# Kernel tuning notes

Measured on AMD Instinct MI355X. Metric: run time of the kernel, lower is better.

The kernel has to match this reference:

```python
import jax, jax.numpy as jnp
import numpy as np

N, E = 50000, 1000000
IN_DIM, HID, OUT = 2, 32, 16
H1, H2 = 4, 1
NEG_SLOPE = 0.2
LN_EPS = 1e-5


def _glorot(key, shape):
    fan_in, fan_out = shape[0], shape[1]
    lim = (6.0 / (fan_in + fan_out)) ** 0.5
    return jax.random.uniform(key, shape, jnp.float32, -lim, lim)


def layer_norm(x, g, b):
    mu = jnp.mean(x, axis=-1, keepdims=True)
    var = jnp.var(x, axis=-1, keepdims=True)
    return (x - mu) * jax.lax.rsqrt(var + LN_EPS) * g + b


def gatv2_conv(x, src, dst, edge_attr, Wl, bl, Wr, br, We, att, bias, H, C):
    # x: (N, F) -> out: (N, C)  (concat=False: mean over heads)
    n = x.shape[0]
    xl = (x @ Wl + bl).reshape(n, H, C)   # source transform
    xr = (x @ Wr + br).reshape(n, H, C)   # destination transform
    e = (edge_attr @ We).reshape(-1, H, C)  # edge feature transform (no bias)
    # per-edge message, LeakyReLU, attention logit
    m = jax.nn.leaky_relu(xl[src] + xr[dst] + e, NEG_SLOPE)  # (E, H, C)
    logit = jnp.einsum('ehc,hc->eh', m, att)                 # (E, H)
    # scatter softmax grouped by destination node
    amax = jax.ops.segment_max(logit, dst, num_segments=n)    # (N, H)
    ex = jnp.exp(logit - amax[dst])                           # (E, H)
    denom = jax.ops.segment_sum(ex, dst, num_segments=n)      # (N, H)
    alpha = ex / (denom[dst] + 1e-16)                         # (E, H)
    # weighted scatter-aggregate of source features
    out = jax.ops.segment_sum(alpha[:, :, None] * xl[src], dst, num_segments=n)  # (N, H, C)
    return jnp.mean(out, axis=1) + bias


def setup_inputs() -> dict:
    key = jax.random.key(0)
    ks = jax.random.split(key, 16)
    x = jax.random.normal(ks[0], (N, IN_DIM), jnp.float32)
    edge_index = jax.random.randint(ks[1], (2, E), 0, N, jnp.int64)
    edge_attr = jax.random.normal(ks[2], (E, 1), jnp.float32)
    inp = {
        'x': x, 'edge_index': edge_index, 'edge_attr': edge_attr,
        # layer 1 (in=2 -> H1*HID)
        'W1l': _glorot(ks[3], (IN_DIM, H1 * HID)), 'b1l': jnp.zeros((H1 * HID,), jnp.float32),
        'W1r': _glorot(ks[4], (IN_DIM, H1 * HID)), 'b1r': jnp.zeros((H1 * HID,), jnp.float32),
        'We1': _glorot(ks[5], (1, H1 * HID)),
        'att1': _glorot(ks[6], (H1, HID)),
        'bias1': jnp.zeros((HID,), jnp.float32),
        'g1': jnp.ones((HID,), jnp.float32), 'beta1': jnp.zeros((HID,), jnp.float32),
        # layer 2 (HID -> H2*OUT)
        'W2l': _glorot(ks[7], (HID, H2 * OUT)), 'b2l': jnp.zeros((H2 * OUT,), jnp.float32),
        'W2r': _glorot(ks[8], (HID, H2 * OUT)), 'b2r': jnp.zeros((H2 * OUT,), jnp.float32),
        'We2': _glorot(ks[9], (1, H2 * OUT)),
        'att2': _glorot(ks[10], (H2, OUT)),
        'bias2': jnp.zeros((OUT,), jnp.float32),
        'g2': jnp.ones((OUT,), jnp.float32), 'beta2': jnp.zeros((OUT,), jnp.float32),
    }
    return inp


def reference(x, edge_index, edge_attr, W1l, b1l, W1r, b1r, We1, att1, bias1, g1, beta1,
              W2l, b2l, W2r, b2r, We2, att2, bias2, g2, beta2):
    src, dst = edge_index[0], edge_index[1]
    h = gatv2_conv(x, src, dst, edge_attr, W1l, b1l, W1r, b1r, We1, att1, bias1, H1, HID)
    h = jax.nn.elu(layer_norm(h, g1, beta1))  # dropout p=0.0 -> identity
    z = gatv2_conv(h, src, dst, edge_attr, W2l, b2l, W2r, b2r, We2, att2, bias2, H2, OUT)
    return layer_norm(z, g2, beta2)
```

## Files before the change

kernel.cpp:

```cpp
#include <hip/hip_runtime.h>
#include <hip/hip_bf16.h>
#include <math.h>

typedef __hip_bfloat16 bf16;

__device__ __forceinline__ float b2f(bf16 v) { return __bfloat162float(v); }
__device__ __forceinline__ bf16  f2b(float v) { return __float2bfloat16(v); }

template<int F32>
__device__ __forceinline__ float ldf(const void* p, int i) {
    return F32 ? ((const float*)p)[i] : b2f(((const bf16*)p)[i]);
}
template<int F32>
__device__ __forceinline__ void ldx(const void* x, int s, float& x0, float& x1) {
    if (F32) { float2 v = ((const float2*)x)[s]; x0 = v.x; x1 = v.y; }
    else {
        unsigned u = ((const unsigned*)x)[s];
        x0 = __uint_as_float((u & 0xFFFFu) << 16);
        x1 = __uint_as_float(u & 0xFFFF0000u);
    }
}
__device__ __forceinline__ unsigned f2b_hi(float f) {
    unsigned u = __float_as_uint(f);
    u += 0x7FFFu + ((u >> 16) & 1u);
    return u & 0xFFFF0000u;
}
template<int P4>
__device__ __forceinline__ void ldrec(const void* csr, int k, int& s, float& a) {
    if (P4) {
        unsigned u = ((const unsigned*)csr)[k];
        s = (int)(u & 0xFFFFu);
        a = __uint_as_float(u & 0xFFFF0000u);
    } else {
        uint2 r = ((const uint2*)csr)[k];
        s = (int)r.x;
        a = __uint_as_float(r.y);
    }
}
__device__ __forceinline__ float sclamp(float v, float lim) {
    return fminf(fmaxf(v, -lim), lim);
}
template<int CTRL>
__device__ __forceinline__ float dpp_add(float v) {
    int t = __builtin_amdgcn_update_dpp(0, __float_as_int(v), CTRL, 0xF, 0xF, true);
    return v + __int_as_float(t);
}
__device__ __forceinline__ float red16(float v) {
    v = dpp_add<0xB1>(v);
    v = dpp_add<0x4E>(v);
    v = dpp_add<0x124>(v);
    v = dpp_add<0x128>(v);
    return v;
}

#define NEG_SLOPE 0.2f
#define LN_EPS 1e-5f
#define SCAN_TILE 1024
#define ACHUNK 2048
#define EBMAX 512

__device__ __forceinline__ int ld_idx(const int* ei, long long pos, int is64, int N) {
    int v = is64 ? ei[2 * pos] : ei[pos];
    return min(max(v, 0), N - 1);
}
__device__ __forceinline__ int calc_is64(const int* ei) {
    int hi = 0, nz = 0;
    #pragma unroll
    for (int i = 0; i < 8; ++i) { hi |= ei[2 * i + 1]; nz |= ei[2 * i]; }
    return (hi == 0 && nz != 0) ? 1 : 0;
}
__device__ __forceinline__ int calc_isf32(const unsigned short* xu) {
    int pl = 0;
    for (int i = 0; i < 32; ++i) {
        unsigned ex = (xu[2 * i] >> 7) & 0xFF;
        if (ex >= 100 && ex <= 140) pl++;
    }
    return (pl >= 24) ? 0 : 1;
}


template<int F32>
__device__ void bina1_body(const int* __restrict__ ei, const void* __restrict__ attr,
                           int E, int N, int is64,
                           uint2* __restrict__ binned, int* __restrict__ cntm,
                           int* __restrict__ locm,
                           int* cnt, int* incl, int* cur, uint2* stage) {
    int tid = threadIdx.x, b = blockIdx.x;
    cnt[tid] = 0;
    __syncthreads();
    int i0 = b * ACHUNK;
    int iend = min(i0 + ACHUNK, E);
    uint2 rec[8]; int bk[8];
    #pragma unroll
    for (int r = 0; r < 8; ++r) {
        int i = i0 + tid + r * 256;
        bk[r] = -1;
        if (i < iend) {
            int d = ld_idx(ei, (long long)E + i, is64, N);
            int s = ld_idx(ei, (long long)i, is64, N);
            float a = ldf<F32>(attr, i);
            rec[r] = make_uint2((unsigned)s | ((unsigned)(d & 255) << 16), f2b_hi(a));
            bk[r] = d >> 8;
            atomicAdd(&cnt[bk[r]], 1);
        }
    }
    __syncthreads();
    incl[tid] = cnt[tid];
    __syncthreads();
    for (int off = 1; off < 256; off <<= 1) {
        int u = (tid >= off) ? incl[tid - off] : 0;
        __syncthreads();
        incl[tid] += u;
        __syncthreads();
    }
    cur[tid] = incl[tid] - cnt[tid];
    __syncthreads();
    #pragma unroll
    for (int r = 0; r < 8; ++r) {
        if (bk[r] >= 0) {
            int p = atomicAdd(&cur[bk[r]], 1);
            stage[p] = rec[r];
        }
    }
    __syncthreads();
    int n = iend - i0;
    for (int i = tid; i < n; i += 256)
        binned[(size_t)b * ACHUNK + i] = stage[i];
    cntm[b * 256 + tid] = cnt[tid];
    locm[b * 256 + tid] = incl[tid] - cnt[tid];
}

__global__ __launch_bounds__(256) void bina1_kernel(const int* __restrict__ ei,
                                                    const void* __restrict__ attr,
                                                    const unsigned short* __restrict__ xu,
                                                    int E, int N, int* __restrict__ flags,
                                                    uint2* __restrict__ binned,
                                                    int* __restrict__ cntm,
                                                    int* __restrict__ locm) {
    __shared__ int cnt[256], incl[256], cur[256];
    __shared__ uint2 stage[ACHUNK];
    __shared__ int sflags[2];
    if (threadIdx.x == 0) {
        sflags[0] = calc_is64(ei);
        sflags[1] = calc_isf32(xu);
        if (blockIdx.x == 0) { flags[0] = sflags[0]; flags[1] = sflags[1]; }
    }
    __syncthreads();
    if (sflags[1]) bina1_body<1>(ei, attr, E, N, sflags[0], binned, cntm, locm,
                                 cnt, incl, cur, stage);
    else           bina1_body<0>(ei, attr, E, N, sflags[0], binned, cntm, locm,
                                 cnt, incl, cur, stage);
}

__global__ __launch_bounds__(256) void sumb_kernel(const int* __restrict__ cntm,
                                                   int* __restrict__ btot, int EB) {
    __shared__ int w[4];
    int B = blockIdx.x, tid = threadIdx.x;
    int s = 0;
    for (int j = tid; j < EB; j += 256) s += cntm[j * 256 + B];
    #pragma unroll
    for (int off = 1; off < 64; off <<= 1) s += __shfl_xor(s, off);
    if ((tid & 63) == 0) w[tid >> 6] = s;
    __syncthreads();
    if (tid == 0) btot[B] = w[0] + w[1] + w[2] + w[3];
}

__global__ void scanc_kernel(const int* __restrict__ btot, int* __restrict__ bbase,
                             int* __restrict__ rowptr, int NB, int N, int E) {
    __shared__ int s[256];
    int tid = threadIdx.x;
    int v = (tid < NB) ? btot[tid] : 0;
    s[tid] = v;
    __syncthreads();
    for (int off = 1; off < 256; off <<= 1) {
        int u = (tid >= off) ? s[tid - off] : 0;
        __syncthreads();
        s[tid] += u;
        __syncthreads();
    }
    if (tid < NB) bbase[tid] = s[tid] - v;
    if (tid == 0) { bbase[NB] = s[255]; rowptr[N] = E; }
}

__global__ __launch_bounds__(256) void passb_kernel(const uint2* __restrict__ binned,
                                                    const int* __restrict__ cntm,
                                                    const int* __restrict__ locm,
                                                    const int* __restrict__ bbase,
                                                    int* __restrict__ rowptr,
                                                    unsigned* __restrict__ csr,
                                                    int N, int EB) {
    __shared__ int nc[256], incl[256], cur[256];
    __shared__ int cntl[EBMAX], locl[EBMAX];
    int B = blockIdx.x, tid = threadIdx.x;
    for (int j = tid; j < EB; j += 256) {
        cntl[j] = cntm[j * 256 + B];
        locl[j] = locm[j * 256 + B];
    }
    nc[tid] = 0;
    __syncthreads();
    for (int j = tid; j < EB; j += 256) {
        int c = cntl[j];
        const uint2* src = binned + (size_t)j * ACHUNK + locl[j];
        for (int i = 0; i < c; ++i)
            atomicAdd(&nc[(src[i].x >> 16) & 255], 1);
    }
    __syncthreads();
    incl[tid] = nc[tid];
    __syncthreads();
    for (int off = 1; off < 256; off <<= 1) {
        int u = (tid >= off) ? incl[tid - off] : 0;
        __syncthreads();
        incl[tid] += u;
        __syncthreads();
    }
    int base = bbase[B];
    int excl = incl[tid] - nc[tid];
    int node = (B << 8) + tid;
    if (node < N) rowptr[node] = base + excl;
    cur[tid] = excl;
    __syncthreads();
    for (int j = tid; j < EB; j += 256) {
        int c = cntl[j];
        const uint2* src = binned + (size_t)j * ACHUNK + locl[j];
        for (int i = 0; i < c; ++i) {
            uint2 r = src[i];
            int p = atomicAdd(&cur[(r.x >> 16) & 255], 1);
            csr[base + p] = r.y | (r.x & 0xFFFFu);
        }
    }
}


__global__ void hist_kernel(const int* __restrict__ ei, const unsigned short* __restrict__ xu,
                            int E, int N, int* __restrict__ flags, int* __restrict__ cnt) {
    int is64 = calc_is64(ei);
    if (blockIdx.x == 0 && threadIdx.x == 0) {
        flags[0] = is64;
        flags[1] = calc_isf32(xu);
    }
    int e = blockIdx.x * blockDim.x + threadIdx.x;
    if (e >= E) return;
    atomicAdd(&cnt[ld_idx(ei, (long long)E + e, is64, N)], 1);
}

__global__ __launch_bounds__(256) void scan_partial(const int* __restrict__ cnt,
                                                    int* __restrict__ bsum, int N) {
    __shared__ int wsum[4];
    int b = blockIdx.x, tid = threadIdx.x;
    int base = b * SCAN_TILE + tid * 4;
    int4 v = make_int4(0, 0, 0, 0);
    if (base + 3 < N) v = *(const int4*)(cnt + base);
    else {
        if (base + 0 < N) v.x = cnt[base + 0];
        if (base + 1 < N) v.y = cnt[base + 1];
        if (base + 2 < N) v.z = cnt[base + 2];
    }
    int s = v.x + v.y + v.z + v.w;
    #pragma unroll
    for (int off = 1; off < 64; off <<= 1) s += __shfl_xor(s, off);
    if ((tid & 63) == 0) wsum[tid >> 6] = s;
    __syncthreads();
    if (tid == 0) bsum[b] = wsum[0] + wsum[1] + wsum[2] + wsum[3];
}

__global__ __launch_bounds__(256) void scan_final(int* __restrict__ cnt, int* __restrict__ rowptr,
                                                  const int* __restrict__ bsum, int N, int B) {
    __shared__ int tsum[256];
    __shared__ int bpre[256];
    int b = blockIdx.x, tid = threadIdx.x;
    bpre[tid] = (tid < B) ? bsum[tid] : 0;
    int base = b * SCAN_TILE + tid * 4;
    int4 v = make_int4(0, 0, 0, 0);
    if (base + 3 < N) v = *(const int4*)(cnt + base);
    else {
        if (base + 0 < N) v.x = cnt[base + 0];
        if (base + 1 < N) v.y = cnt[base + 1];
        if (base + 2 < N) v.z = cnt[base + 2];
    }
    tsum[tid] = v.x + v.y + v.z + v.w;
    __syncthreads();
    for (int off = 1; off < 256; off <<= 1) {
        int t = (tid >= off) ? tsum[tid - off] : 0;
        int u = (tid >= off) ? bpre[tid - off] : 0;
        __syncthreads();
        tsum[tid] += t;
        bpre[tid] += u;
        __syncthreads();
    }
    int blockpre = (b == 0) ? 0 : bpre[b - 1];
    int o0 = blockpre + ((tid == 0) ? 0 : tsum[tid - 1]);
    int o1 = o0 + v.x, o2 = o1 + v.y, o3 = o2 + v.z;
    if (base + 3 < N) {
        int4 o = make_int4(o0, o1, o2, o3);
        *(int4*)(rowptr + base) = o;
        *(int4*)(cnt + base) = o;
    } else {
        if (base + 0 < N) { rowptr[base + 0] = o0; cnt[base + 0] = o0; }
        if (base + 1 < N) { rowptr[base + 1] = o1; cnt[base + 1] = o1; }
        if (base + 2 < N) { rowptr[base + 2] = o2; cnt[base + 2] = o2; }
    }
    if (b == 0 && tid == 255) rowptr[N] = bpre[255];
}

template<int F32>
__device__ void scatter_body(const int* __restrict__ ei, const void* __restrict__ attr,
                             int E, int N, int is64, int* __restrict__ cursor,
                             uint2* __restrict__ csr) {
    int e = blockIdx.x * blockDim.x + threadIdx.x;
    if (e >= E) return;
    int d = ld_idx(ei, (long long)E + e, is64, N);
    int s = ld_idx(ei, (long long)e, is64, N);
    float av = ldf<F32>(attr, e);
    int pos = atomicAdd(&cursor[d], 1);
    csr[pos] = make_uint2((unsigned)s, __float_as_uint(av));
}

__global__ void scatter_kernel(const int* __restrict__ ei, const void* __restrict__ attr,
                               int E, int N, const int* __restrict__ flags,
                               int* __restrict__ cursor, uint2* __restrict__ csr) {
    if (flags[1]) scatter_body<1>(ei, attr, E, N, flags[0], cursor, csr);
    else          scatter_body<0>(ei, attr, E, N, flags[0], cursor, csr);
}


template<int F32, int P4>
__device__ void agg1_body(
    const int* __restrict__ rowptr, const void* __restrict__ csr,
    const void* __restrict__ x,
    const void* W1l, const void* b1l, const void* W1r, const void* b1r,
    const void* We1, const void* att1, const void* bias1, const void* g1v, const void* beta1,
    bf16* __restrict__ hout, int N) {
    int w0 = __builtin_amdgcn_readfirstlane((blockIdx.x * blockDim.x + threadIdx.x) >> 6);
    int NW = (gridDim.x * blockDim.x) >> 6;
    int lane = threadIdx.x & 63;
    int h = lane >> 4, q = lane & 15;
    int ja = h * 32 + q, jb = ja + 16;

    float wlaA = ldf<F32>(W1l, ja),      wlaB = ldf<F32>(W1l, jb);
    float wlbA = ldf<F32>(W1l, 128 + ja), wlbB = ldf<F32>(W1l, 128 + jb);
    float wraA = ldf<F32>(W1r, ja),      wraB = ldf<F32>(W1r, jb);
    float wrbA = ldf<F32>(W1r, 128 + ja), wrbB = ldf<F32>(W1r, 128 + jb);
    float blA = ldf<F32>(b1l, ja), blB = ldf<F32>(b1l, jb);
    float brA = ldf<F32>(b1r, ja), brB = ldf<F32>(b1r, jb);
    float weA = ldf<F32>(We1, ja), weB = ldf<F32>(We1, jb);
    float atA = ldf<F32>(att1, ja), atB = ldf<F32>(att1, jb);
    float aa4A = 0.4f * atA, aa4B = 0.4f * atB;
    float blbrA = blA + brA, blbrB = blB + brB;
    float P0 = 0.6f * red16(atA * wlaA + atB * wlaB);
    float P1 = 0.6f * red16(atA * wlbA + atB * wlbB);
    float Pw = 0.6f * red16(atA * weA + atB * weB);
    float Q0 = 0.6f * red16(atA * wraA + atB * wraB);
    float Q1 = 0.6f * red16(atA * wrbA + atB * wrbB);
    float Qc = 0.6f * red16(atA * blbrA + atB * blbrB);
    float biasA = ldf<F32>(bias1, q), biasB = ldf<F32>(bias1, q + 16);
    float gA = ldf<F32>(g1v, q), gB = ldf<F32>(g1v, q + 16);
    float beA = ldf<F32>(beta1, q), beB = ldf<F32>(beta1, q + 16);

    for (int n = w0; n < N; n += NW) {
        int beg = rowptr[n], end = rowptr[n + 1];
        float xd0, xd1;
        ldx<F32>(x, n, xd0, xd1);
        float cA = fmaf(xd0, wraA, fmaf(xd1, wrbA, blbrA));
        float cB = fmaf(xd0, wraB, fmaf(xd1, wrbB, blbrB));
        float Kn = fmaf(xd0, Q0, fmaf(xd1, Q1, Qc));
        float S = 0.f, Sx0 = 0.f, Sx1 = 0.f;

        auto edge = [&](float xs0, float xs1, float a) {
            float zA = fmaf(xs0, wlaA, fmaf(xs1, wlbA, fmaf(a, weA, cA)));
            float zB = fmaf(xs0, wlaB, fmaf(xs1, wlbB, fmaf(a, weB, cB)));
            float pabs = red16(fmaf(fabsf(zA), aa4A, fabsf(zB) * aa4B));
            float p = sclamp(fmaf(xs0, P0, fmaf(xs1, P1, fmaf(a, Pw, Kn))) + pabs, 60.f);
            float e = __expf(p);
            S += e;
            Sx0 = fmaf(e, xs0, Sx0);
            Sx1 = fmaf(e, xs1, Sx1);
        };

        int k = beg;
        for (; k + 4 <= end; k += 4) {
            int s0, s1, s2, s3;
            float a0, a1, a2, a3;
            ldrec<P4>(csr, k, s0, a0);
            ldrec<P4>(csr, k + 1, s1, a1);
            ldrec<P4>(csr, k + 2, s2, a2);
            ldrec<P4>(csr, k + 3, s3, a3);
            float p0, p1, q0, q1, r0, r1, t0, t1;
            ldx<F32>(x, s0, p0, p1);
            ldx<F32>(x, s1, q0, q1);
            ldx<F32>(x, s2, r0, r1);
            ldx<F32>(x, s3, t0, t1);
            edge(p0, p1, a0);
            edge(q0, q1, a1);
            edge(r0, r1, a2);
            edge(t0, t1, a3);
        }
        for (; k < end; ++k) {
            int s0; float a0;
            ldrec<P4>(csr, k, s0, a0);
            float p0, p1;
            ldx<F32>(x, s0, p0, p1);
            edge(p0, p1, a0);
        }

        float inv = 1.0f / (S + 1e-16f);
        float R = S * inv, U0 = Sx0 * inv, U1 = Sx1 * inv;
        float outA = fmaf(U0, wlaA, fmaf(U1, wlbA, R * blA));
        float outB = fmaf(U0, wlaB, fmaf(U1, wlbB, R * blB));
        outA += __shfl_xor(outA, 16); outA += __shfl_xor(outA, 32);
        outB += __shfl_xor(outB, 16); outB += __shfl_xor(outB, 32);
        float valA = fmaf(0.25f, outA, biasA);
        float valB = fmaf(0.25f, outB, biasB);
        float mu = red16(valA + valB) * (1.f / 32.f);
        float dA = valA - mu, dB = valB - mu;
        float var = red16(dA * dA + dB * dB) * (1.f / 32.f);
        float rs = rsqrtf(var + LN_EPS);
        float yA = fmaf(dA * rs, gA, beA);
        float yB = fmaf(dB * rs, gB, beB);
        float hA = yA > 0.f ? yA : expm1f(yA);
        float hB = yB > 0.f ? yB : expm1f(yB);
        if (lane < 16) {
            hout[n * 32 + q]      = f2b(hA);
            hout[n * 32 + 16 + q] = f2b(hB);
        }
    }
}

template<int P4>
__global__ __launch_bounds__(256) void agg1_kernel(
    const int* __restrict__ flags,
    const int* __restrict__ rowptr, const void* __restrict__ csr,
    const void* __restrict__ x,
    const void* W1l, const void* b1l, const void* W1r, const void* b1r,
    const void* We1, const void* att1, const void* bias1, const void* g1v, const void* beta1,
    bf16* __restrict__ hout, int N) {
    if (flags[1]) agg1_body<1, P4>(rowptr, csr, x, W1l, b1l, W1r, b1r,
                                   We1, att1, bias1, g1v, beta1, hout, N);
    else          agg1_body<0, P4>(rowptr, csr, x, W1l, b1l, W1r, b1r,
                                   We1, att1, bias1, g1v, beta1, hout, N);
}


template<int F32>
__device__ void node2_body(bf16* __restrict__ hbuf, float* wl, float* wr,
                           const void* W2l, const void* b2l, const void* W2r, const void* b2r,
                           int N) {
    __shared__ float bl[16], br[16];
    int tid = threadIdx.x;
    for (int i = tid; i < 512; i += 256) { wl[i] = ldf<F32>(W2l, i); wr[i] = ldf<F32>(W2r, i); }
    if (tid < 16) { bl[tid] = ldf<F32>(b2l, tid); br[tid] = ldf<F32>(b2r, tid); }
    __syncthreads();
    int n = blockIdx.x * blockDim.x + tid;
    if (n >= N) return;
    float hv[32];
    #pragma unroll
    for (int c = 0; c < 32; ++c) hv[c] = b2f(hbuf[n * 32 + c]);
    float accl[16], accr[16];
    #pragma unroll
    for (int o = 0; o < 16; ++o) { accl[o] = bl[o]; accr[o] = br[o]; }
    #pragma unroll
    for (int c = 0; c < 32; ++c) {
        #pragma unroll
        for (int o = 0; o < 16; ++o) {
            accl[o] = fmaf(hv[c], wl[c * 16 + o], accl[o]);
            accr[o] = fmaf(hv[c], wr[c * 16 + o], accr[o]);
        }
    }
    #pragma unroll
    for (int o = 0; o < 16; ++o) {
        hbuf[n * 32 + o]      = f2b(accl[o]);
        hbuf[n * 32 + 16 + o] = f2b(accr[o]);
    }
}

__global__ __launch_bounds__(256) void node2_kernel(
    const int* __restrict__ flags, bf16* __restrict__ hbuf,
    const void* W2l, const void* b2l, const void* W2r, const void* b2r, int N) {
    __shared__ float wl[512], wr[512];
    if (flags[1]) node2_body<1>(hbuf, wl, wr, W2l, b2l, W2r, b2r, N);
    else          node2_body<0>(hbuf, wl, wr, W2l, b2l, W2r, b2r, N);
}


template<int F32, int P4>
__device__ void agg2_body(
    const int* __restrict__ rowptr, const void* __restrict__ csr,
    const bf16* __restrict__ h2,
    const void* We2, const void* att2, const void* bias2, const void* g2v, const void* beta2,
    void* __restrict__ out, int N) {
    int w0 = __builtin_amdgcn_readfirstlane((blockIdx.x * blockDim.x + threadIdx.x) >> 6);
    int NW = (gridDim.x * blockDim.x) >> 6;
    int lane = threadIdx.x & 63;
    int g = lane >> 4, t = lane & 15;

    float we = ldf<F32>(We2, t), at = ldf<F32>(att2, t);
    float bia = ldf<F32>(bias2, t), gg = ldf<F32>(g2v, t), bb = ldf<F32>(beta2, t);

    for (int n = w0; n < N; n += NW) {
        int beg = rowptr[n], end = rowptr[n + 1];
        float xr = b2f(h2[n * 32 + 16 + t]);

        float S = 0.f, A = 0.f;
        auto edge = [&](float v, float a) {
            float m = fmaf(a, we, v + xr);
            m = fmaxf(m, NEG_SLOPE * m);
            float p = sclamp(red16(m * at), 60.f);
            float e = __expf(p);
            S += e;
            A = fmaf(e, v, A);
        };
        int k = beg + g;
        for (; k + 4 < end; k += 8) {
            int s0, s1; float a0, a1;
            ldrec<P4>(csr, k, s0, a0);
            ldrec<P4>(csr, k + 4, s1, a1);
            float v0 = b2f(h2[s0 * 32 + t]);
            float v1 = b2f(h2[s1 * 32 + t]);
            edge(v0, a0);
            edge(v1, a1);
        }
        if (k < end) {
            int s0; float a0;
            ldrec<P4>(csr, k, s0, a0);
            edge(b2f(h2[s0 * 32 + t]), a0);
        }
        S += __shfl_xor(S, 16); S += __shfl_xor(S, 32);
        A += __shfl_xor(A, 16); A += __shfl_xor(A, 32);
        float val = A / (S + 1e-16f) + bia;

        float mu = red16(val) * (1.f / 16.f);
        float d = val - mu;
        float var = red16(d * d) * (1.f / 16.f);
        float y = fmaf(d * rsqrtf(var + LN_EPS), gg, bb);
        if (lane < 16) {
            if (F32) ((float*)out)[n * 16 + t] = y;
            else     ((bf16*)out)[n * 16 + t] = f2b(y);
        }
    }
}

template<int P4>
__global__ __launch_bounds__(256) void agg2_kernel(
    const int* __restrict__ flags,
    const int* __restrict__ rowptr, const void* __restrict__ csr,
    const bf16* __restrict__ h2,
    const void* We2, const void* att2, const void* bias2, const void* g2v, const void* beta2,
    void* __restrict__ out, int N) {
    if (flags[1]) agg2_body<1, P4>(rowptr, csr, h2, We2, att2, bias2, g2v, beta2, out, N);
    else          agg2_body<0, P4>(rowptr, csr, h2, We2, att2, bias2, g2v, beta2, out, N);
}


static inline size_t align256(size_t x) { return (x + 255) & ~size_t(255); }

extern "C" void kernel_launch(void* const* d_in, const int* in_sizes, int n_in,
                              void* d_out, int out_size, void* d_ws, size_t ws_size,
                              hipStream_t stream) {
    const void* x     = d_in[0];
    const int*  ei    = (const int*)d_in[1];
    const void* eattr = d_in[2];
    const void* W1l   = d_in[3];
    const void* b1l   = d_in[4];
    const void* W1r   = d_in[5];
    const void* b1r   = d_in[6];
    const void* We1   = d_in[7];
    const void* att1  = d_in[8];
    const void* bias1 = d_in[9];
    const void* g1    = d_in[10];
    const void* beta1 = d_in[11];
    const void* W2l   = d_in[12];
    const void* b2l   = d_in[13];
    const void* W2r   = d_in[14];
    const void* b2r   = d_in[15];
    const void* We2   = d_in[16];
    const void* att2  = d_in[17];
    const void* bias2 = d_in[18];
    const void* g2    = d_in[19];
    const void* beta2 = d_in[20];

    const int N = in_sizes[0] / 2;
    const int E = in_sizes[2];
    const int EB = (E + ACHUNK - 1) / ACHUNK;
    const int NB = (N + 255) >> 8;
    const bool p4 = (N <= 65536) && (EB <= EBMAX);

    char* ws = (char*)d_ws;
    size_t off = 0;
    int* flags  = (int*)(ws + off); off += align256(sizeof(int) * 2);
    int* cntm   = (int*)(ws + off); off += align256(sizeof(int) * (size_t)EB * 256);
    int* locm   = (int*)(ws + off); off += align256(sizeof(int) * (size_t)EB * 256);
    int* btot   = (int*)(ws + off); off += align256(sizeof(int) * 256);
    int* bbase  = (int*)(ws + off); off += align256(sizeof(int) * 257);
    int* rowptr = (int*)(ws + off); off += align256(sizeof(int) * (size_t)(N + 1));
    void* csr   = (void*)(ws + off); off += align256((p4 ? 4u : 8u) * (size_t)E);
    char* big   = (ws + off);
    uint2* binned = (uint2*)big;
    bf16*  hbuf   = (bf16*)big;

    if (p4) {
        bina1_kernel<<<EB, 256, 0, stream>>>(ei, eattr, (const unsigned short*)x,
                                             E, N, flags, binned, cntm, locm);
        sumb_kernel<<<NB, 256, 0, stream>>>(cntm, btot, EB);
        scanc_kernel<<<1, 256, 0, stream>>>(btot, bbase, rowptr, NB, N, E);
        passb_kernel<<<NB, 256, 0, stream>>>(binned, cntm, locm, bbase, rowptr,
                                             (unsigned*)csr, N, EB);
    } else {
        int* cnt = (int*)big;
        hbuf = (bf16*)(big + align256(sizeof(int) * (size_t)N));
        const int B = (N + SCAN_TILE - 1) / SCAN_TILE;
        hipMemsetAsync(cnt, 0, sizeof(int) * (size_t)N, stream);
        hist_kernel<<<(E + 255) / 256, 256, 0, stream>>>(ei, (const unsigned short*)x, E, N, flags, cnt);
        scan_partial<<<B, 256, 0, stream>>>(cnt, cntm, N);
        scan_final<<<B, 256, 0, stream>>>(cnt, rowptr, cntm, N, B);
        scatter_kernel<<<(E + 255) / 256, 256, 0, stream>>>(ei, eattr, E, N, flags, cnt, (uint2*)csr);
    }

    if (p4) agg1_kernel<1><<<2048, 256, 0, stream>>>(flags, rowptr, csr, x,
                                                     W1l, b1l, W1r, b1r, We1, att1,
                                                     bias1, g1, beta1, hbuf, N);
    else    agg1_kernel<0><<<2048, 256, 0, stream>>>(flags, rowptr, csr, x,
                                                     W1l, b1l, W1r, b1r, We1, att1,
                                                     bias1, g1, beta1, hbuf, N);

    node2_kernel<<<(N + 255) / 256, 256, 0, stream>>>(flags, hbuf, W2l, b2l, W2r, b2r, N);

    if (p4) agg2_kernel<1><<<2048, 256, 0, stream>>>(flags, rowptr, csr, hbuf,
                                                     We2, att2, bias2, g2, beta2, d_out, N);
    else    agg2_kernel<0><<<2048, 256, 0, stream>>>(flags, rowptr, csr, hbuf,
                                                     We2, att2, bias2, g2, beta2, d_out, N);
}
```

Before: 219.0 us.

## Split binned records into packed words plus byte keys and stage per-bucket in LDS

The intermediate binned edge records shrink from 8 bytes to a 4-byte packed source/attr word plus a separate 1-byte low-destination key. The single-block scan kernel is removed: each passb block now scans the bucket totals itself, and sumb writes rowptr[N]. When a bucket fits in shared memory (up to 8192 edges), passb reads its edges from global memory once into LDS and does the counting and final scatter from LDS, instead of reading the binned data twice. This cuts global traffic and one launch, at the cost of a larger LDS footprint per block and a fallback path for oversized buckets.

```diff
diff --git a/kernel.cpp b/kernel.cpp
--- a/kernel.cpp
+++ b/kernel.cpp
@@ -58,6 +58,7 @@
 #define SCAN_TILE 1024
 #define ACHUNK 2048
 #define EBMAX 512
+#define SCAP 8192
 
 __device__ __forceinline__ int ld_idx(const int* ei, long long pos, int is64, int N) {
     int v = is64 ? ei[2 * pos] : ei[pos];
@@ -82,15 +83,16 @@
 template<int F32>
 __device__ void bina1_body(const int* __restrict__ ei, const void* __restrict__ attr,
                            int E, int N, int is64,
-                           uint2* __restrict__ binned, int* __restrict__ cntm,
-                           int* __restrict__ locm,
-                           int* cnt, int* incl, int* cur, uint2* stage) {
+                           unsigned* __restrict__ binned4, unsigned char* __restrict__ binnedb,
+                           int* __restrict__ cntm, int* __restrict__ locm,
+                           int* cnt, int* incl, int* cur,
+                           unsigned* stage4, unsigned char* stageb) {
     int tid = threadIdx.x, b = blockIdx.x;
     cnt[tid] = 0;
     __syncthreads();
     int i0 = b * ACHUNK;
     int iend = min(i0 + ACHUNK, E);
-    uint2 rec[8]; int bk[8];
+    unsigned rec[8]; int bk[8], lo[8];
     #pragma unroll
     for (int r = 0; r < 8; ++r) {
         int i = i0 + tid + r * 256;
@@ -99,8 +101,9 @@
             int d = ld_idx(ei, (long long)E + i, is64, N);
             int s = ld_idx(ei, (long long)i, is64, N);
             float a = ldf<F32>(attr, i);
-            rec[r] = make_uint2((unsigned)s | ((unsigned)(d & 255) << 16), f2b_hi(a));
+            rec[r] = f2b_hi(a) | (unsigned)s;
             bk[r] = d >> 8;
+            lo[r] = d & 255;
             atomicAdd(&cnt[bk[r]], 1);
         }
     }
@@ -119,13 +122,16 @@
     for (int r = 0; r < 8; ++r) {
         if (bk[r] >= 0) {
             int p = atomicAdd(&cur[bk[r]], 1);
-            stage[p] = rec[r];
+            stage4[p] = rec[r];
+            stageb[p] = (unsigned char)lo[r];
         }
     }
     __syncthreads();
     int n = iend - i0;
-    for (int i = tid; i < n; i += 256)
-        binned[(size_t)b * ACHUNK + i] = stage[i];
+    for (int i = tid; i < n; i += 256) {
+        binned4[(size_t)b * ACHUNK + i] = stage4[i];
+        binnedb[(size_t)b * ACHUNK + i] = stageb[i];
+    }
     cntm[b * 256 + tid] = cnt[tid];
     locm[b * 256 + tid] = incl[tid] - cnt[tid];
 }
@@ -134,11 +140,13 @@
                                                     const void* __restrict__ attr,
                                                     const unsigned short* __restrict__ xu,
                                                     int E, int N, int* __restrict__ flags,
-                                                    uint2* __restrict__ binned,
+                                                    unsigned* __restrict__ binned4,
+                                                    unsigned char* __restrict__ binnedb,
                                                     int* __restrict__ cntm,
                                                     int* __restrict__ locm) {
     __shared__ int cnt[256], incl[256], cur[256];
-    __shared__ uint2 stage[ACHUNK];
+    __shared__ unsigned stage4[ACHUNK];
+    __shared__ unsigned char stageb[ACHUNK];
     __shared__ int sflags[2];
     if (threadIdx.x == 0) {
         sflags[0] = calc_is64(ei);
@@ -146,16 +154,18 @@
         if (blockIdx.x == 0) { flags[0] = sflags[0]; flags[1] = sflags[1]; }
     }
     __syncthreads();
-    if (sflags[1]) bina1_body<1>(ei, attr, E, N, sflags[0], binned, cntm, locm,
-                                 cnt, incl, cur, stage);
-    else           bina1_body<0>(ei, attr, E, N, sflags[0], binned, cntm, locm,
-                                 cnt, incl, cur, stage);
+    if (sflags[1]) bina1_body<1>(ei, attr, E, N, sflags[0], binned4, binnedb, cntm, locm,
+                                 cnt, incl, cur, stage4, stageb);
+    else           bina1_body<0>(ei, attr, E, N, sflags[0], binned4, binnedb, cntm, locm,
+                                 cnt, incl, cur, stage4, stageb);
 }
 
 __global__ __launch_bounds__(256) void sumb_kernel(const int* __restrict__ cntm,
-                                                   int* __restrict__ btot, int EB) {
+                                                   int* __restrict__ btot, int EB,
+                                                   int* __restrict__ rowptr, int N, int E) {
     __shared__ int w[4];
     int B = blockIdx.x, tid = threadIdx.x;
+    if (B == 0 && tid == 0) rowptr[N] = E;
     int s = 0;
     for (int j = tid; j < EB; j += 256) s += cntm[j * 256 + B];
     #pragma unroll
@@ -165,44 +175,63 @@
     if (tid == 0) btot[B] = w[0] + w[1] + w[2] + w[3];
 }
 
-__global__ void scanc_kernel(const int* __restrict__ btot, int* __restrict__ bbase,
-                             int* __restrict__ rowptr, int NB, int N, int E) {
-    __shared__ int s[256];
-    int tid = threadIdx.x;
-    int v = (tid < NB) ? btot[tid] : 0;
-    s[tid] = v;
-    __syncthreads();
-    for (int off = 1; off < 256; off <<= 1) {
-        int u = (tid >= off) ? s[tid - off] : 0;
-        __syncthreads();
-        s[tid] += u;
-        __syncthreads();
-    }
-    if (tid < NB) bbase[tid] = s[tid] - v;
-    if (tid == 0) { bbase[NB] = s[255]; rowptr[N] = E; }
-}
-
-__global__ __launch_bounds__(256) void passb_kernel(const uint2* __restrict__ binned,
+__global__ __launch_bounds__(256) void passb_kernel(const unsigned* __restrict__ binned4,
+                                                    const unsigned char* __restrict__ binnedb,
                                                     const int* __restrict__ cntm,
                                                     const int* __restrict__ locm,
-                                                    const int* __restrict__ bbase,
+                                                    const int* __restrict__ btot,
                                                     int* __restrict__ rowptr,
                                                     unsigned* __restrict__ csr,
-                                                    int N, int EB) {
-    __shared__ int nc[256], incl[256], cur[256];
+                                                    int N, int EB, int NB) {
+    __shared__ int nc[256], incl[256], cur[256], bsc[256], ebase[256];
     __shared__ int cntl[EBMAX], locl[EBMAX];
+    __shared__ unsigned stage4[SCAP];
+    __shared__ unsigned char stageb[SCAP];
+    __shared__ int stageCnt;
     int B = blockIdx.x, tid = threadIdx.x;
+    int v = (tid < NB) ? btot[tid] : 0;
+    bsc[tid] = v;
+    nc[tid] = 0;
+    if (tid == 0) stageCnt = 0;
     for (int j = tid; j < EB; j += 256) {
         cntl[j] = cntm[j * 256 + B];
         locl[j] = locm[j * 256 + B];
     }
-    nc[tid] = 0;
-    __syncthreads();
-    for (int j = tid; j < EB; j += 256) {
-        int c = cntl[j];
-        const uint2* src = binned + (size_t)j * ACHUNK + locl[j];
-        for (int i = 0; i < c; ++i)
-            atomicAdd(&nc[(src[i].x >> 16) & 255], 1);
+    __syncthreads();
+    for (int off = 1; off < 256; off <<= 1) {
+        int u = (tid >= off) ? bsc[tid - off] : 0;
+        __syncthreads();
+        bsc[tid] += u;
+        __syncthreads();
+    }
+    ebase[tid] = bsc[tid] - v;
+    __syncthreads();
+    int base = ebase[B];
+    int cntb = btot[B];
+    bool fit = (cntb <= SCAP);
+
+    if (fit) {
+        for (int j = tid; j < EB; j += 256) {
+            int c = cntl[j];
+            if (c > 0) {
+                int p = atomicAdd(&stageCnt, c);
+                const unsigned* s4 = binned4 + (size_t)j * ACHUNK + locl[j];
+                const unsigned char* sb = binnedb + (size_t)j * ACHUNK + locl[j];
+                for (int i = 0; i < c; ++i) {
+                    unsigned r4 = s4[i];
+                    unsigned char l = sb[i];
+                    stage4[p + i] = r4;
+                    stageb[p + i] = l;
+                    atomicAdd(&nc[l], 1);
+                }
+            }
+        }
+    } else {
+        for (int j = tid; j < EB; j += 256) {
+            int c = cntl[j];
+            const unsigned char* sb = binnedb + (size_t)j * ACHUNK + locl[j];
+            for (int i = 0; i < c; ++i) atomicAdd(&nc[sb[i]], 1);
+        }
     }
     __syncthreads();
     incl[tid] = nc[tid];
@@ -213,19 +242,26 @@
         incl[tid] += u;
         __syncthreads();
     }
-    int base = bbase[B];
     int excl = incl[tid] - nc[tid];
     int node = (B << 8) + tid;
     if (node < N) rowptr[node] = base + excl;
     cur[tid] = excl;
     __syncthreads();
-    for (int j = tid; j < EB; j += 256) {
-        int c = cntl[j];
-        const uint2* src = binned + (size_t)j * ACHUNK + locl[j];
-        for (int i = 0; i < c; ++i) {
-            uint2 r = src[i];
-            int p = atomicAdd(&cur[(r.x >> 16) & 255], 1);
-            csr[base + p] = r.y | (r.x & 0xFFFFu);
+    if (fit) {
+        for (int i = tid; i < cntb; i += 256) {
+            int l = stageb[i];
+            int p = atomicAdd(&cur[l], 1);
+            csr[base + p] = stage4[i];
+        }
+    } else {
+        for (int j = tid; j < EB; j += 256) {
+            int c = cntl[j];
+            const unsigned* s4 = binned4 + (size_t)j * ACHUNK + locl[j];
+            const unsigned char* sb = binnedb + (size_t)j * ACHUNK + locl[j];
+            for (int i = 0; i < c; ++i) {
+                int p = atomicAdd(&cur[sb[i]], 1);
+                csr[base + p] = s4[i];
+            }
         }
     }
 }
@@ -589,20 +625,19 @@
     int* cntm   = (int*)(ws + off); off += align256(sizeof(int) * (size_t)EB * 256);
     int* locm   = (int*)(ws + off); off += align256(sizeof(int) * (size_t)EB * 256);
     int* btot   = (int*)(ws + off); off += align256(sizeof(int) * 256);
-    int* bbase  = (int*)(ws + off); off += align256(sizeof(int) * 257);
     int* rowptr = (int*)(ws + off); off += align256(sizeof(int) * (size_t)(N + 1));
     void* csr   = (void*)(ws + off); off += align256((p4 ? 4u : 8u) * (size_t)E);
     char* big   = (ws + off);
-    uint2* binned = (uint2*)big;
-    bf16*  hbuf   = (bf16*)big;
+    unsigned* binned4 = (unsigned*)big;
+    unsigned char* binnedb = (unsigned char*)(big + align256(sizeof(unsigned) * (size_t)EB * ACHUNK));
+    bf16* hbuf = (bf16*)big;
 
     if (p4) {
         bina1_kernel<<<EB, 256, 0, stream>>>(ei, eattr, (const unsigned short*)x,
-                                             E, N, flags, binned, cntm, locm);
-        sumb_kernel<<<NB, 256, 0, stream>>>(cntm, btot, EB);
-        scanc_kernel<<<1, 256, 0, stream>>>(btot, bbase, rowptr, NB, N, E);
-        passb_kernel<<<NB, 256, 0, stream>>>(binned, cntm, locm, bbase, rowptr,
-                                             (unsigned*)csr, N, EB);
+                                             E, N, flags, binned4, binnedb, cntm, locm);
+        sumb_kernel<<<NB, 256, 0, stream>>>(cntm, btot, EB, rowptr, N, E);
+        passb_kernel<<<NB, 256, 0, stream>>>(binned4, binnedb, cntm, locm, btot,
+                                             rowptr, (unsigned*)csr, N, EB, NB);
     } else {
         int* cnt = (int*)big;
         hbuf = (bf16*)(big + align256(sizeof(int) * (size_t)N));
```

Result: faster. 209.3 us (median of 2 runs) (-4.5%).
